# Performance work log

Hardware: AMD Instinct MI355X
Metric: run time of the kernel (lower is better)

## Reference

```python
import jax, jax.numpy as jnp
import numpy as np

DIM = 256
N_EMBED = 8192
BETA = 0.25


def setup_inputs() -> dict:
    key = jax.random.key(0)
    k1, k2, k3, k4 = jax.random.split(key, 4)
    inp = {
        "input": jax.random.normal(k1, (16, 1024, DIM), dtype=jnp.float32),
        # nn.Embedding weight init: normal(0, dim**-0.5)
        "embed_weight": jax.random.normal(k2, (N_EMBED, DIM), dtype=jnp.float32) * (DIM ** -0.5),
        # nn.Linear(dim, dim): weight [out, in], bias [out]
        "proj_w": jax.random.normal(k3, (DIM, DIM), dtype=jnp.float32) * (DIM ** -0.5),
        "proj_b": jax.random.normal(k4, (DIM,), dtype=jnp.float32) * 0.01,
    }
    return inp


def reference(input, embed_weight, proj_w, proj_b):
    flatten = input.reshape(-1, DIM)                      # [N, d]
    # projected codebook: Linear(embedding.weight)
    quant_codebook = embed_weight @ proj_w.T + proj_b     # [K, d]
    d = (jnp.sum(flatten ** 2, axis=1, keepdims=True)
         + jnp.sum(quant_codebook ** 2, axis=1)
         - 2.0 * jnp.einsum('nd,kd->nk', flatten, quant_codebook))  # [N, K]
    min_encoding_indices = jnp.argmin(d, axis=1)          # [N]
    z_quantize = quant_codebook[min_encoding_indices].reshape(input.shape)
    sg = jax.lax.stop_gradient
    diff = jnp.mean((sg(z_quantize) - input) ** 2)
    commit_loss = jnp.mean((z_quantize - sg(input)) ** 2)
    diff = diff + BETA * commit_loss                      # legacy=True branch
    # straight-through estimator
    z_quantize = input + sg(z_quantize - input)
    return (z_quantize, diff, min_encoding_indices)
```

## Files before the change

### kernel.cpp

```cpp
#include <hip/hip_runtime.h>

#define DIMD   256
#define NTOK   16384
#define NCODE  8192
#define NELEM  (NTOK * DIMD)

#define BM 128
#define BK 128
#define BD 32
#define PAD 4
#define LDS_STRIDE (BM + PAD)

#define SPLITS_B 4
#define CODES_PER_WAVE (NCODE / SPLITS_B / 4)
#define NGROUPS (CODES_PER_WAVE / 16)
#define MARGIN 0.5f
#define EBUF_CAP 1024

#define PROJ_BLOCKS ((NCODE / BM) * (DIMD / BK))
#define CONV_BLOCKS (NTOK / 4)

typedef float floatx4 __attribute__((ext_vector_type(4)));
typedef short short8  __attribute__((ext_vector_type(8)));

__device__ __forceinline__ unsigned short f2bf(float f) {
    unsigned u = __float_as_uint(f);
    unsigned r = (u + 0x7FFFu + ((u >> 16) & 1u)) >> 16;
    return (unsigned short)r;
}

__device__ __forceinline__ unsigned fkey(float f) {
    unsigned u = __float_as_uint(f);
    return (u & 0x80000000u) ? ~u : (u | 0x80000000u);
}
__device__ __forceinline__ float funkey(unsigned k) {
    unsigned u = (k & 0x80000000u) ? (k & 0x7FFFFFFFu) : ~k;
    return __uint_as_float(u);
}

__device__ __forceinline__ size_t cb2_idx(int row, int col) {
    return ((size_t)((row >> 4) * 8 + (col >> 5))) * 512
         + (size_t)((((col >> 3) & 3) * 16 + (row & 15)) * 8 + (col & 7));
}

__global__ __launch_bounds__(256, 3)
void prep_kernel(const float* __restrict__ E, const float* __restrict__ W,
                 const float* __restrict__ bias, float* __restrict__ C,
                 unsigned short* __restrict__ Cb2,
                 float* __restrict__ cnormA, float* __restrict__ cnormB,
                 const float* __restrict__ X, float* __restrict__ xnorm,
                 unsigned short* __restrict__ Xb,
                 unsigned long long* __restrict__ fin,
                 unsigned* __restrict__ minkey,
                 unsigned* __restrict__ cnt, float* __restrict__ out)
{
    __shared__ float smem[2 * BD * LDS_STRIDE];

    const int bid = blockIdx.x;
    const int tid = threadIdx.x;

    if (bid >= PROJ_BLOCKS) {
        const int row0 = (bid - PROJ_BLOCKS) * 4;
        const int wave = tid >> 6;
        const int lane = tid & 63;
        const int row  = row0 + wave;
        float4 v = *(const float4*)&X[(size_t)row * DIMD + lane * 4];
        ushort4 h = {f2bf(v.x), f2bf(v.y), f2bf(v.z), f2bf(v.w)};
        *(ushort4*)&Xb[(size_t)row * DIMD + lane * 4] = h;
        float s = v.x * v.x + v.y * v.y + v.z * v.z + v.w * v.w;
#pragma unroll
        for (int off = 1; off < 64; off <<= 1) s += __shfl_xor(s, off);
        if (lane == 0) xnorm[row] = s;
        if (tid < 4) {
            fin[row0 + tid]    = ~0ull;
            minkey[row0 + tid] = ~0u;
        }
        if (bid == PROJ_BLOCKS && tid == 0) { *cnt = 0; out[NELEM] = 0.f; }
        return;
    }

    float* As = smem;
    float* Bs = smem + BD * LDS_STRIDE;

    const int tx  = tid & 15;
    const int ty  = tid >> 4;
    const int m0  = (bid & 63) * BM;
    const int j0  = (bid >> 6) * BK;

    const int srow = tid >> 3;
    const int scol = (tid & 7) * 4;

    float acc[8][8];
#pragma unroll
    for (int i = 0; i < 8; ++i)
#pragma unroll
        for (int j = 0; j < 8; ++j) acc[i][j] = 0.f;

    for (int dc = 0; dc < DIMD / BD; ++dc) {
        const int d0 = dc * BD;
        __syncthreads();
#pragma unroll
        for (int rr = 0; rr < 4; ++rr) {
            const int r = srow + rr * 32;
            float4 av = *(const float4*)&E[(size_t)(m0 + r) * DIMD + d0 + scol];
            As[(scol + 0) * LDS_STRIDE + r] = av.x;
            As[(scol + 1) * LDS_STRIDE + r] = av.y;
            As[(scol + 2) * LDS_STRIDE + r] = av.z;
            As[(scol + 3) * LDS_STRIDE + r] = av.w;
            float4 bv = *(const float4*)&W[(size_t)(j0 + r) * DIMD + d0 + scol];
            Bs[(scol + 0) * LDS_STRIDE + r] = bv.x;
            Bs[(scol + 1) * LDS_STRIDE + r] = bv.y;
            Bs[(scol + 2) * LDS_STRIDE + r] = bv.z;
            Bs[(scol + 3) * LDS_STRIDE + r] = bv.w;
        }
        __syncthreads();
#pragma unroll 4
        for (int d = 0; d < BD; ++d) {
            float4 a0 = *(float4*)&As[d * LDS_STRIDE + ty * 4];
            float4 a1 = *(float4*)&As[d * LDS_STRIDE + 64 + ty * 4];
            float4 b0 = *(float4*)&Bs[d * LDS_STRIDE + tx * 4];
            float4 b1 = *(float4*)&Bs[d * LDS_STRIDE + 64 + tx * 4];
            float a[8] = {a0.x, a0.y, a0.z, a0.w, a1.x, a1.y, a1.z, a1.w};
            float b[8] = {b0.x, b0.y, b0.z, b0.w, b1.x, b1.y, b1.z, b1.w};
#pragma unroll
            for (int i = 0; i < 8; ++i)
#pragma unroll
                for (int j = 0; j < 8; ++j) acc[i][j] = fmaf(a[i], b[j], acc[i][j]);
        }
    }

    __syncthreads();
    float* red = smem;

    float4 bja = *(const float4*)&bias[j0 + tx * 4];
    float4 bjb = *(const float4*)&bias[j0 + 64 + tx * 4];
#pragma unroll
    for (int i = 0; i < 8; ++i) {
        const int mloc = (i < 4) ? (ty * 4 + i) : (64 + ty * 4 + (i - 4));
        const int row  = m0 + mloc;
        const size_t rbase = (size_t)row * DIMD;
        float o[8] = {acc[i][0] + bja.x, acc[i][1] + bja.y, acc[i][2] + bja.z, acc[i][3] + bja.w,
                      acc[i][4] + bjb.x, acc[i][5] + bjb.y, acc[i][6] + bjb.z, acc[i][7] + bjb.w};
        *(float4*)&C[rbase + j0 + tx * 4]      = *(float4*)&o[0];
        *(float4*)&C[rbase + j0 + 64 + tx * 4] = *(float4*)&o[4];
        ushort4 h0 = {f2bf(o[0]), f2bf(o[1]), f2bf(o[2]), f2bf(o[3])};
        ushort4 h1 = {f2bf(o[4]), f2bf(o[5]), f2bf(o[6]), f2bf(o[7])};
        *(ushort4*)&Cb2[cb2_idx(row, j0 + tx * 4)]      = h0;
        *(ushort4*)&Cb2[cb2_idx(row, j0 + 64 + tx * 4)] = h1;
        float p = 0.f;
#pragma unroll
        for (int j = 0; j < 8; ++j) p = fmaf(o[j], o[j], p);
        red[mloc * 16 + tx] = p;
    }
    __syncthreads();
    if (tid < 128) {
        float s = 0.f;
#pragma unroll
        for (int k = 0; k < 16; ++k) s += red[tid * 16 + k];
        float* dst = (j0 == 0) ? cnormA : cnormB;
        dst[m0 + tid] = s;
    }
}

__global__ __launch_bounds__(256, 2)
void dist_min_kernel(const unsigned short* __restrict__ Xb,
                     const unsigned short* __restrict__ Cb2,
                     const float* __restrict__ cnormA,
                     const float* __restrict__ cnormB,
                     unsigned* __restrict__ minkey)
{
    __shared__ float wmin[4][64];

    const int tid  = threadIdx.x;
    const int lane = tid & 63;
    const int wv   = tid >> 6;
    const int l15  = lane & 15;
    const int quad = lane >> 4;
    const int tok0 = blockIdx.x * 64;
    const int cbase = blockIdx.y * (NCODE / SPLITS_B) + wv * CODES_PER_WAVE;

    short8 a[4][8];
#pragma unroll
    for (int i = 0; i < 4; ++i) {
        const unsigned short* ap = Xb + (size_t)(tok0 + i * 16 + l15) * DIMD + quad * 8;
#pragma unroll
        for (int ks = 0; ks < 8; ++ks)
            a[i][ks] = *(const short8*)(ap + ks * 32);
    }

    float runv[16];
#pragma unroll
    for (int s = 0; s < 16; ++s) runv[s] = 3.4e38f;

    const unsigned short* bp0 = Cb2 + (size_t)cbase * DIMD + lane * 8;

    short8 breg[2][8];
    float  cnr[2];
#pragma unroll
    for (int ks = 0; ks < 8; ++ks) breg[0][ks] = *(const short8*)(bp0 + ks * 512);
    cnr[0] = cnormA[cbase + l15] + cnormB[cbase + l15];

    auto group_body = [&](int g, short8 (&bc)[8], short8 (&bn)[8],
                          float cnc, float& cnn) {
        if (g + 1 < NGROUPS) {
            const unsigned short* bpn = bp0 + (size_t)(g + 1) * 4096;
#pragma unroll
            for (int ks = 0; ks < 8; ++ks) bn[ks] = *(const short8*)(bpn + ks * 512);
            const int cnx = cbase + (g + 1) * 16 + l15;
            cnn = cnormA[cnx] + cnormB[cnx];
        }

        floatx4 acc[4];
#pragma unroll
        for (int i = 0; i < 4; ++i) acc[i] = (floatx4){0.f, 0.f, 0.f, 0.f};
#pragma unroll
        for (int ks = 0; ks < 8; ++ks)
#pragma unroll
            for (int i = 0; i < 4; ++i)
                acc[i] = __builtin_amdgcn_mfma_f32_16x16x32_bf16(a[i][ks], bc[ks], acc[i], 0, 0, 0);

#pragma unroll
        for (int i = 0; i < 4; ++i)
#pragma unroll
            for (int r = 0; r < 4; ++r)
                runv[i * 4 + r] = fminf(runv[i * 4 + r], fmaf(-2.f, acc[i][r], cnc));
    };

    for (int gg = 0; gg < NGROUPS; gg += 2) {
        group_body(gg,     breg[0], breg[1], cnr[0], cnr[1]);
        group_body(gg + 1, breg[1], breg[0], cnr[1], cnr[0]);
    }

#pragma unroll
    for (int s = 0; s < 16; ++s) {
        float m = runv[s];
#pragma unroll
        for (int off = 1; off < 16; off <<= 1) m = fminf(m, __shfl_xor(m, off));
        runv[s] = m;
    }
    if (l15 == 0) {
#pragma unroll
        for (int i = 0; i < 4; ++i)
#pragma unroll
            for (int r = 0; r < 4; ++r)
                wmin[wv][i * 16 + quad * 4 + r] = runv[i * 4 + r];
    }
    __syncthreads();
    if (tid < 64) {
        const float bm = fminf(fminf(wmin[0][tid], wmin[1][tid]),
                               fminf(wmin[2][tid], wmin[3][tid]));
        atomicMin(&minkey[tok0 + tid], fkey(bm));
    }
}

__global__ __launch_bounds__(256, 2)
void dist_emit_kernel(const unsigned short* __restrict__ Xb,
                      const unsigned short* __restrict__ Cb2,
                      const float* __restrict__ cnormA,
                      const float* __restrict__ cnormB,
                      const unsigned* __restrict__ minkey,
                      unsigned* __restrict__ list, unsigned* __restrict__ count,
                      unsigned cap)
{
    __shared__ float tokthr[64];
    __shared__ unsigned ebuf[EBUF_CAP];
    __shared__ unsigned ecnt, gbase;

    const int tid  = threadIdx.x;
    const int lane = tid & 63;
    const int wv   = tid >> 6;
    const int l15  = lane & 15;
    const int quad = lane >> 4;
    const int tok0 = blockIdx.x * 64;
    const int cbase = blockIdx.y * (NCODE / SPLITS_B) + wv * CODES_PER_WAVE;

    if (tid == 0) ecnt = 0;
    if (tid < 64) tokthr[tid] = funkey(minkey[tok0 + tid]) + MARGIN;
    __syncthreads();

    short8 a[4][8];
#pragma unroll
    for (int i = 0; i < 4; ++i) {
        const unsigned short* ap = Xb + (size_t)(tok0 + i * 16 + l15) * DIMD + quad * 8;
#pragma unroll
        for (int ks = 0; ks < 8; ++ks)
            a[i][ks] = *(const short8*)(ap + ks * 32);
    }

    float thr[16];
#pragma unroll
    for (int i = 0; i < 4; ++i)
#pragma unroll
        for (int r = 0; r < 4; ++r)
            thr[i * 4 + r] = tokthr[i * 16 + quad * 4 + r];

    const unsigned short* bp0 = Cb2 + (size_t)cbase * DIMD + lane * 8;

    short8 breg[2][8];
    float  cnr[2];
#pragma unroll
    for (int ks = 0; ks < 8; ++ks) breg[0][ks] = *(const short8*)(bp0 + ks * 512);
    cnr[0] = cnormA[cbase + l15] + cnormB[cbase + l15];

    auto group_body = [&](int g, short8 (&bc)[8], short8 (&bn)[8],
                          float cnc, float& cnn) {
        const int code0 = cbase + g * 16;
        if (g + 1 < NGROUPS) {
            const unsigned short* bpn = bp0 + (size_t)(g + 1) * 4096;
#pragma unroll
            for (int ks = 0; ks < 8; ++ks) bn[ks] = *(const short8*)(bpn + ks * 512);
            const int cnx = code0 + 16 + l15;
            cnn = cnormA[cnx] + cnormB[cnx];
        }

        floatx4 acc[4];
#pragma unroll
        for (int i = 0; i < 4; ++i) acc[i] = (floatx4){0.f, 0.f, 0.f, 0.f};
#pragma unroll
        for (int ks = 0; ks < 8; ++ks)
#pragma unroll
            for (int i = 0; i < 4; ++i)
                acc[i] = __builtin_amdgcn_mfma_f32_16x16x32_bf16(a[i][ks], bc[ks], acc[i], 0, 0, 0);

        unsigned mask = 0;
#pragma unroll
        for (int i = 0; i < 4; ++i)
#pragma unroll
            for (int r = 0; r < 4; ++r) {
                const float dd = fmaf(-2.f, acc[i][r], cnc);
                if (dd < thr[i * 4 + r]) mask |= (1u << (i * 4 + r));
            }

        if (__any(mask != 0)) {
            if (mask) {
                unsigned pos = atomicAdd(&ecnt, (unsigned)__popc(mask));
#pragma unroll
                for (int i = 0; i < 4; ++i)
#pragma unroll
                    for (int r = 0; r < 4; ++r) {
                        const int s = i * 4 + r;
                        if (mask & (1u << s)) {
                            const unsigned token = tok0 + i * 16 + quad * 4 + r;
                            const unsigned entry = (token << 13) | (unsigned)(code0 + l15);
                            if (pos < EBUF_CAP) ebuf[pos] = entry;
                            else { unsigned gp = atomicAdd(count, 1u); if (gp < cap) list[gp] = entry; }
                            ++pos;
                        }
                    }
            }
        }
    };

    for (int gg = 0; gg < NGROUPS; gg += 2) {
        group_body(gg,     breg[0], breg[1], cnr[0], cnr[1]);
        group_body(gg + 1, breg[1], breg[0], cnr[1], cnr[0]);
    }

    __syncthreads();
    const unsigned n = (ecnt < EBUF_CAP) ? ecnt : EBUF_CAP;
    if (tid == 0) gbase = atomicAdd(count, n);
    __syncthreads();
    const unsigned gb = gbase;
    for (unsigned i = tid; i < n; i += 256) {
        const unsigned p = gb + i;
        if (p < cap) list[p] = ebuf[i];
    }
}

__global__ __launch_bounds__(256)
void rescore_kernel(const float* __restrict__ X, const float* __restrict__ C,
                    const float* __restrict__ xnorm,
                    const float* __restrict__ cnormA,
                    const float* __restrict__ cnormB,
                    const unsigned* __restrict__ list, const unsigned* __restrict__ count,
                    unsigned cap, unsigned long long* __restrict__ fin)
{
    const int lane = threadIdx.x & 63;
    const int g16  = lane & 15;
    const int sub  = lane >> 4;
    const int gid  = ((blockIdx.x * 256 + threadIdx.x) >> 6) * 4 + sub;
    const int ng   = ((gridDim.x * 256) >> 6) * 4;
    unsigned n = *count; if (n > cap) n = cap;

    for (unsigned c = gid; c < n; c += ng) {
        const unsigned e = list[c];
        const unsigned tok = e >> 13, code = e & 8191u;
        const float* xr = &X[(size_t)tok * DIMD];
        const float* cr = &C[(size_t)code * DIMD];
        float dot = 0.f;
#pragma unroll
        for (int r = 0; r < 4; ++r) {
            float4 x4 = *(const float4*)&xr[r * 64 + g16 * 4];
            float4 c4 = *(const float4*)&cr[r * 64 + g16 * 4];
            dot = fmaf(x4.x, c4.x, dot);
            dot = fmaf(x4.y, c4.y, dot);
            dot = fmaf(x4.z, c4.z, dot);
            dot = fmaf(x4.w, c4.w, dot);
        }
#pragma unroll
        for (int d = 1; d < 16; d <<= 1) dot += __shfl_xor(dot, d);
        if (g16 == 0) {
            const float dd = xnorm[tok] + (cnormA[code] + cnormB[code]) - 2.f * dot;
            const unsigned long long p =
                ((unsigned long long)__float_as_uint(dd) << 32) | code;
            atomicMin(&fin[tok], p);
        }
    }
}

__global__ __launch_bounds__(256)
void finalize_kernel(const float* __restrict__ X, const float* __restrict__ C,
                     const unsigned long long* __restrict__ fin,
                     float* __restrict__ out)
{
    __shared__ float part[4];
    const int lane = threadIdx.x & 63;
    const int wv   = threadIdx.x >> 6;
    const int t0   = blockIdx.x * 64;

    float local = 0.f;
    for (int it = 0; it < 16; ++it) {
        const int t = t0 + wv * 16 + it;
        const unsigned code = (unsigned)(fin[t] & 0xFFFFFFFFull);
        float4 c4 = *(const float4*)&C[(size_t)code * DIMD + lane * 4];
        float4 x4 = *(const float4*)&X[(size_t)t * DIMD + lane * 4];
        float4 w  = {c4.x - x4.x, c4.y - x4.y, c4.z - x4.z, c4.w - x4.w};
        local += w.x * w.x + w.y * w.y + w.z * w.z + w.w * w.w;
        float4 zq = {x4.x + w.x, x4.y + w.y, x4.z + w.z, x4.w + w.w};
        *(float4*)&out[(size_t)t * DIMD + lane * 4] = zq;
        if (lane == 0) out[NELEM + 1 + t] = (float)code;
    }
#pragma unroll
    for (int off = 1; off < 64; off <<= 1) local += __shfl_xor(local, off);
    if (lane == 0) part[wv] = local;
    __syncthreads();
    if (threadIdx.x == 0) {
        const float s = part[0] + part[1] + part[2] + part[3];
        atomicAdd(&out[NELEM], s * (1.25f / (float)NELEM));
    }
}

extern "C" void kernel_launch(void* const* d_in, const int* in_sizes, int n_in,
                              void* d_out, int out_size, void* d_ws, size_t ws_size,
                              hipStream_t stream)
{
    const float* X = (const float*)d_in[0];
    const float* E = (const float*)d_in[1];
    const float* W = (const float*)d_in[2];
    const float* b = (const float*)d_in[3];
    float* out = (float*)d_out;

    char* w = (char*)d_ws;
    float* C            = (float*)w;           w += (size_t)NCODE * DIMD * 4;
    unsigned short* Xb  = (unsigned short*)w;  w += (size_t)NTOK * DIMD * 2;
    unsigned short* Cb2 = (unsigned short*)w;  w += (size_t)NCODE * DIMD * 2;
    float* xnorm        = (float*)w;           w += (size_t)NTOK * 4;
    float* cnormA       = (float*)w;           w += (size_t)NCODE * 4;
    float* cnormB       = (float*)w;           w += (size_t)NCODE * 4;
    unsigned* cnt       = (unsigned*)w;        w += 256;
    unsigned long long* fin = (unsigned long long*)w; w += (size_t)NTOK * 8;
    unsigned* minkey    = (unsigned*)w;        w += (size_t)NTOK * 4;
    unsigned* list      = (unsigned*)w;

    size_t used = (size_t)(w - (char*)d_ws);
    size_t avail = (ws_size > used) ? (ws_size - used) / 4 : 0;
    unsigned cap = (unsigned)((avail > 16777216u) ? 16777216u : avail);

    prep_kernel<<<PROJ_BLOCKS + CONV_BLOCKS, 256, 0, stream>>>(
        E, W, b, C, Cb2, cnormA, cnormB, X, xnorm, Xb, fin, minkey, cnt, out);
    dist_min_kernel<<<dim3(NTOK / 64, SPLITS_B), 256, 0, stream>>>(
        Xb, Cb2, cnormA, cnormB, minkey);
    dist_emit_kernel<<<dim3(NTOK / 64, SPLITS_B), 256, 0, stream>>>(
        Xb, Cb2, cnormA, cnormB, minkey, list, cnt, cap);
    rescore_kernel<<<1024, 256, 0, stream>>>(X, C, xnorm, cnormA, cnormB, list, cnt, cap, fin);
    finalize_kernel<<<NTOK / 64, 256, 0, stream>>>(X, C, fin, out);
}
```

Before: 278.2 us.

## Share codebook tiles across waves via async global-to-LDS double buffering

Restructures the distance kernels so each block covers 256 tokens (64 per wave) against a 1024-code slice. Codebook tiles are staged once per block into double-buffered LDS with global_load_lds and shared by all four waves, instead of each wave streaming its own codes into registers. Code norms are also precomputed into LDS. This cuts redundant global/L2 traffic for the codebook. The cost is a __syncthreads per 16-code group, which serializes the waves, plus per-lane atomicMin calls on minkey in place of the old block-level reduction.

```diff
diff --git a/kernel.cpp b/kernel.cpp
--- a/kernel.cpp
+++ b/kernel.cpp
@@ -11,9 +11,9 @@
 #define PAD 4
 #define LDS_STRIDE (BM + PAD)
 
-#define SPLITS_B 4
-#define CODES_PER_WAVE (NCODE / SPLITS_B / 4)
-#define NGROUPS (CODES_PER_WAVE / 16)
+#define CODES_PER_BLOCK 1024
+#define TOK_PER_BLOCK   256
+#define NGROUPS (CODES_PER_BLOCK / 16)
 #define MARGIN 0.5f
 #define EBUF_CAP 1024
 
@@ -22,11 +22,18 @@
 
 typedef float floatx4 __attribute__((ext_vector_type(4)));
 typedef short short8  __attribute__((ext_vector_type(8)));
+typedef unsigned int u32;
 
 __device__ __forceinline__ unsigned short f2bf(float f) {
     unsigned u = __float_as_uint(f);
     unsigned r = (u + 0x7FFFu + ((u >> 16) & 1u)) >> 16;
     return (unsigned short)r;
+}
+
+__device__ __forceinline__ void gl_lds16(const void* g, void* l) {
+    __builtin_amdgcn_global_load_lds(
+        (const __attribute__((address_space(1))) u32*)g,
+        (__attribute__((address_space(3))) u32*)l, 16, 0, 0);
 }
 
 __device__ __forceinline__ unsigned fkey(float f) {
@@ -169,15 +176,36 @@
                      const float* __restrict__ cnormB,
                      unsigned* __restrict__ minkey)
 {
-    __shared__ float wmin[4][64];
+    __shared__ short Bls[2][4096];
+    __shared__ float cnl[CODES_PER_BLOCK];
 
     const int tid  = threadIdx.x;
     const int lane = tid & 63;
     const int wv   = tid >> 6;
     const int l15  = lane & 15;
     const int quad = lane >> 4;
-    const int tok0 = blockIdx.x * 64;
-    const int cbase = blockIdx.y * (NCODE / SPLITS_B) + wv * CODES_PER_WAVE;
+    const int tok0 = blockIdx.x * TOK_PER_BLOCK + wv * 64;
+    const int cbase = blockIdx.y * CODES_PER_BLOCK;
+
+    {
+        const int t4 = tid * 4;
+        float4 va = *(const float4*)&cnormA[cbase + t4];
+        float4 vb = *(const float4*)&cnormB[cbase + t4];
+        cnl[t4 + 0] = va.x + vb.x;
+        cnl[t4 + 1] = va.y + vb.y;
+        cnl[t4 + 2] = va.z + vb.z;
+        cnl[t4 + 3] = va.w + vb.w;
+    }
+
+    const unsigned short* bsrc = Cb2 + (size_t)cbase * DIMD;
+    auto STAGE = [&](int g) {
+        const unsigned short* s = bsrc + (size_t)g * 4096 + wv * 1024 + lane * 8;
+        short* d = &Bls[g & 1][wv * 1024];
+        gl_lds16(s,       d);
+        gl_lds16(s + 512, d + 512);
+    };
+    STAGE(0);
+    STAGE(1);
 
     short8 a[4][8];
 #pragma unroll
@@ -192,23 +220,14 @@
 #pragma unroll
     for (int s = 0; s < 16; ++s) runv[s] = 3.4e38f;
 
-    const unsigned short* bp0 = Cb2 + (size_t)cbase * DIMD + lane * 8;
-
-    short8 breg[2][8];
-    float  cnr[2];
-#pragma unroll
-    for (int ks = 0; ks < 8; ++ks) breg[0][ks] = *(const short8*)(bp0 + ks * 512);
-    cnr[0] = cnormA[cbase + l15] + cnormB[cbase + l15];
-
-    auto group_body = [&](int g, short8 (&bc)[8], short8 (&bn)[8],
-                          float cnc, float& cnn) {
-        if (g + 1 < NGROUPS) {
-            const unsigned short* bpn = bp0 + (size_t)(g + 1) * 4096;
-#pragma unroll
-            for (int ks = 0; ks < 8; ++ks) bn[ks] = *(const short8*)(bpn + ks * 512);
-            const int cnx = cbase + (g + 1) * 16 + l15;
-            cnn = cnormA[cnx] + cnormB[cnx];
-        }
+    __syncthreads();
+
+    for (int g = 0; g < NGROUPS; ++g) {
+        const short* bp = &Bls[g & 1][lane * 8];
+        short8 bc[8];
+#pragma unroll
+        for (int ks = 0; ks < 8; ++ks) bc[ks] = *(const short8*)(bp + ks * 512);
+        const float cnc = cnl[g * 16 + l15];
 
         floatx4 acc[4];
 #pragma unroll
@@ -224,11 +243,9 @@
 #pragma unroll
             for (int r = 0; r < 4; ++r)
                 runv[i * 4 + r] = fminf(runv[i * 4 + r], fmaf(-2.f, acc[i][r], cnc));
-    };
-
-    for (int gg = 0; gg < NGROUPS; gg += 2) {
-        group_body(gg,     breg[0], breg[1], cnr[0], cnr[1]);
-        group_body(gg + 1, breg[1], breg[0], cnr[1], cnr[0]);
+
+        __syncthreads();
+        if (g + 2 < NGROUPS) STAGE(g + 2);
     }
 
 #pragma unroll
@@ -243,13 +260,7 @@
         for (int i = 0; i < 4; ++i)
 #pragma unroll
             for (int r = 0; r < 4; ++r)
-                wmin[wv][i * 16 + quad * 4 + r] = runv[i * 4 + r];
-    }
-    __syncthreads();
-    if (tid < 64) {
-        const float bm = fminf(fminf(wmin[0][tid], wmin[1][tid]),
-                               fminf(wmin[2][tid], wmin[3][tid]));
-        atomicMin(&minkey[tok0 + tid], fkey(bm));
+                atomicMin(&minkey[tok0 + i * 16 + quad * 4 + r], fkey(runv[i * 4 + r]));
     }
 }
 
@@ -262,7 +273,9 @@
                       unsigned* __restrict__ list, unsigned* __restrict__ count,
                       unsigned cap)
 {
-    __shared__ float tokthr[64];
+    __shared__ short Bls[2][4096];
+    __shared__ float cnl[CODES_PER_BLOCK];
+    __shared__ float tokthr[TOK_PER_BLOCK];
     __shared__ unsigned ebuf[EBUF_CAP];
     __shared__ unsigned ecnt, gbase;
 
@@ -271,12 +284,31 @@
     const int wv   = tid >> 6;
     const int l15  = lane & 15;
     const int quad = lane >> 4;
-    const int tok0 = blockIdx.x * 64;
-    const int cbase = blockIdx.y * (NCODE / SPLITS_B) + wv * CODES_PER_WAVE;
-
+    const int tok0b = blockIdx.x * TOK_PER_BLOCK;
+    const int tok0 = tok0b + wv * 64;
+    const int cbase = blockIdx.y * CODES_PER_BLOCK;
+
+    {
+        const int t4 = tid * 4;
+        float4 va = *(const float4*)&cnormA[cbase + t4];
+        float4 vb = *(const float4*)&cnormB[cbase + t4];
+        cnl[t4 + 0] = va.x + vb.x;
+        cnl[t4 + 1] = va.y + vb.y;
+        cnl[t4 + 2] = va.z + vb.z;
+        cnl[t4 + 3] = va.w + vb.w;
+    }
+    tokthr[tid] = funkey(minkey[tok0b + tid]) + MARGIN;
     if (tid == 0) ecnt = 0;
-    if (tid < 64) tokthr[tid] = funkey(minkey[tok0 + tid]) + MARGIN;
-    __syncthreads();
+
+    const unsigned short* bsrc = Cb2 + (size_t)cbase * DIMD;
+    auto STAGE = [&](int g) {
+        const unsigned short* s = bsrc + (size_t)g * 4096 + wv * 1024 + lane * 8;
+        short* d = &Bls[g & 1][wv * 1024];
+        gl_lds16(s,       d);
+        gl_lds16(s + 512, d + 512);
+    };
+    STAGE(0);
+    STAGE(1);
 
     short8 a[4][8];
 #pragma unroll
@@ -287,31 +319,22 @@
             a[i][ks] = *(const short8*)(ap + ks * 32);
     }
 
+    __syncthreads();
+
     float thr[16];
 #pragma unroll
     for (int i = 0; i < 4; ++i)
 #pragma unroll
         for (int r = 0; r < 4; ++r)
-            thr[i * 4 + r] = tokthr[i * 16 + quad * 4 + r];
-
-    const unsigned short* bp0 = Cb2 + (size_t)cbase * DIMD + lane * 8;
-
-    short8 breg[2][8];
-    float  cnr[2];
-#pragma unroll
-    for (int ks = 0; ks < 8; ++ks) breg[0][ks] = *(const short8*)(bp0 + ks * 512);
-    cnr[0] = cnormA[cbase + l15] + cnormB[cbase + l15];
-
-    auto group_body = [&](int g, short8 (&bc)[8], short8 (&bn)[8],
-                          float cnc, float& cnn) {
+            thr[i * 4 + r] = tokthr[wv * 64 + i * 16 + quad * 4 + r];
+
+    for (int g = 0; g < NGROUPS; ++g) {
         const int code0 = cbase + g * 16;
-        if (g + 1 < NGROUPS) {
-            const unsigned short* bpn = bp0 + (size_t)(g + 1) * 4096;
-#pragma unroll
-            for (int ks = 0; ks < 8; ++ks) bn[ks] = *(const short8*)(bpn + ks * 512);
-            const int cnx = code0 + 16 + l15;
-            cnn = cnormA[cnx] + cnormB[cnx];
-        }
+        const short* bp = &Bls[g & 1][lane * 8];
+        short8 bc[8];
+#pragma unroll
+        for (int ks = 0; ks < 8; ++ks) bc[ks] = *(const short8*)(bp + ks * 512);
+        const float cnc = cnl[g * 16 + l15];
 
         floatx4 acc[4];
 #pragma unroll
@@ -349,11 +372,9 @@
                     }
             }
         }
-    };
-
-    for (int gg = 0; gg < NGROUPS; gg += 2) {
-        group_body(gg,     breg[0], breg[1], cnr[0], cnr[1]);
-        group_body(gg + 1, breg[1], breg[0], cnr[1], cnr[0]);
+
+        __syncthreads();
+        if (g + 2 < NGROUPS) STAGE(g + 2);
     }
 
     __syncthreads();
@@ -468,9 +489,9 @@
 
     prep_kernel<<<PROJ_BLOCKS + CONV_BLOCKS, 256, 0, stream>>>(
         E, W, b, C, Cb2, cnormA, cnormB, X, xnorm, Xb, fin, minkey, cnt, out);
-    dist_min_kernel<<<dim3(NTOK / 64, SPLITS_B), 256, 0, stream>>>(
+    dist_min_kernel<<<dim3(NTOK / TOK_PER_BLOCK, NCODE / CODES_PER_BLOCK), 256, 0, stream>>>(
         Xb, Cb2, cnormA, cnormB, minkey);
-    dist_emit_kernel<<<dim3(NTOK / 64, SPLITS_B), 256, 0, stream>>>(
+    dist_emit_kernel<<<dim3(NTOK / TOK_PER_BLOCK, NCODE / CODES_PER_BLOCK), 256, 0, stream>>>(
         Xb, Cb2, cnormA, cnormB, minkey, list, cnt, cap);
     rescore_kernel<<<1024, 256, 0, stream>>>(X, C, xnorm, cnormA, cnormB, list, cnt, cap, fin);
     finalize_kernel<<<NTOK / 64, 256, 0, stream>>>(X, C, fin, out);
```

Measured after the change: 273.7 us. No clear change (-1.6%).
